# Performance work log

Hardware: AMD Instinct MI355X
Metric: run time of the kernel (lower is better)

The kernel has to match this reference:

```python
import jax, jax.numpy as jnp
import numpy as np

B, S, H, D = 1, 2048, 16, 128
CAUSAL = True


def setup_inputs() -> dict:
    key = jax.random.key(0)
    kq, kk, kv = jax.random.split(key, 3)
    query = jax.random.normal(kq, (B, S, H, D), dtype=jnp.float32)
    k_ = jax.random.normal(kk, (B, S, H, D), dtype=jnp.float32)
    v_ = jax.random.normal(kv, (B, S, H, D), dtype=jnp.float32)
    return {"query": query, "key": k_, "value": v_}


def reference(query, key, value):
    # Single-device equivalent of LongContextAttention:
    # Ulysses all-to-all and ring pass are identity on one rank; the math is
    # standard scaled-dot-product attention with flash-attn's default scale
    # softmax_scale = 1/sqrt(head_dim) and causal masking.
    d = query.shape[-1]
    scale = 1.0 / jnp.sqrt(jnp.asarray(d, dtype=query.dtype))
    # [B,S,H,D] x [B,T,H,D] -> [B,H,S,T]
    scores = jnp.einsum("bshd,bthd->bhst", query, key) * scale
    if CAUSAL:
        s, t = scores.shape[-2], scores.shape[-1]
        mask = jnp.tril(jnp.ones((s, t), dtype=bool))
        scores = jnp.where(mask, scores, jnp.finfo(scores.dtype).min)
    probs = jax.nn.softmax(scores, axis=-1)
    out = jnp.einsum("bhst,bthd->bshd", probs, value)
    return out
```

## Files before the change

### kernel.cpp

```cpp
#include <hip/hip_runtime.h>
#include <hip/hip_bf16.h>
#include <math.h>

#define SS 2048
#define HH 16
#define DD 128
#define HD (HH*DD)
#define QB 128
#define KVB 64

typedef __attribute__((ext_vector_type(8))) short bf16x8;
typedef __attribute__((ext_vector_type(16))) float f32x16;

__device__ __forceinline__ ushort f2bf(float f) {
  __hip_bfloat16 h = __float2bfloat16(f);
  return __builtin_bit_cast(ushort, h);
}
__device__ __forceinline__ uint pk2(float a, float b) {
  return ((uint)f2bf(b) << 16) | (uint)f2bf(a);
}
__device__ __forceinline__ float bf2f(ushort u) {
  uint x = ((uint)u) << 16;
  return __builtin_bit_cast(float, x);
}

__global__ __launch_bounds__(256, 2)
void attn_fwd(const float* __restrict__ Q, const float* __restrict__ K,
              const float* __restrict__ V,
              ushort* __restrict__ PO, float* __restrict__ PM,
              float* __restrict__ PL) {
  __shared__ alignas(16) ushort Klds[2][KVB * DD];
  __shared__ alignas(16) ushort VTlds[2][DD * KVB];

  const int tid  = threadIdx.x;
  const int lane = tid & 63;
  const int wid  = tid >> 6;
  const int q32  = lane & 31;
  const int hi   = lane >> 5;
  const int kxk  = (q32 & 15) << 4;
  const int kxv  = ((q32 & 7) << 4) ^ ((q32 & 8) << 1);

  const int g2   = (tid >> 4) & 3;
  const int n16  = tid & 15;
  const int dstg = wid * 16 + n16;
  const int swv  = ((dstg & 7) << 4) ^ ((dstg & 8) << 1);

  const int bx   = blockIdx.x;
  const int h    = bx & 15;
  const int rest = bx >> 4;
  const int pp   = rest >> 2;
  const int jj   = rest & 3;
  const int LA   = 2 * pp + 2;
  const int BND[5] = {0, 8, 17, 25, 34};
  const int tl = BND[jj], th = BND[jj + 1];

  const float SCALE = 1.44269504088896f / sqrtf((float)DD);
  const float* Kb = K + (size_t)h * DD;
  const float* Vb = V + (size_t)h * DD;

  uint4 kreg[4];
  uint2 vreg[2][4];

  auto loadt = [&](int t0) {
    #pragma unroll
    for (int it = 0; it < 4; ++it) {
      int e = tid + it * 256;
      int row = e >> 4, col = (e & 15) * 8;
      const float* src = &Kb[(size_t)(t0 + row) * HD + col];
      float4 a = *(const float4*)src;
      float4 b = *(const float4*)(src + 4);
      kreg[it].x = pk2(a.x, a.y); kreg[it].y = pk2(a.z, a.w);
      kreg[it].z = pk2(b.x, b.y); kreg[it].w = pk2(b.z, b.w);
    }
    #pragma unroll
    for (int half = 0; half < 2; ++half) {
      const int d = dstg + 64 * half;
      #pragma unroll
      for (int jv = 0; jv < 4; ++jv) {
        const int tt = 16 * jv + 4 * g2;
        const float* vp = &Vb[(size_t)(t0 + tt) * HD + d];
        vreg[half][jv].x = pk2(vp[0],      vp[HD]);
        vreg[half][jv].y = pk2(vp[2 * HD], vp[3 * HD]);
      }
    }
  };
  auto staget = [&](int b) {
    #pragma unroll
    for (int it = 0; it < 4; ++it) {
      int e = tid + it * 256;
      *(uint4*)((char*)&Klds[b][0] + ((e * 16) ^ (e & 0xF0))) = kreg[it];
    }
    #pragma unroll
    for (int half = 0; half < 2; ++half) {
      const int d = dstg + 64 * half;
      #pragma unroll
      for (int jv = 0; jv < 4; ++jv) {
        const int tt = 16 * jv + 4 * g2;
        *(uint2*)((char*)&VTlds[b][0] + ((d * 128 + tt * 2) ^ swv)) = vreg[half][jv];
      }
    }
  };

  for (int phase = 0; phase < 2; ++phase) {
    int qt, lo, hiT;
    if (phase == 0) { qt = pp;      lo = tl;               hiT = min(th, LA); }
    else            { qt = 15 - pp; lo = max(tl, LA) - LA; hiT = th - LA; }
    if (lo >= hiT) continue;

    const int qb = qt * QB;
    const int qw = qb + 32 * wid;
    const int qg = qw + q32;

    bf16x8 qf[8];
    {
      const float* qr = Q + ((size_t)qg * HH + h) * DD;
      #pragma unroll
      for (int ks = 0; ks < 8; ++ks) {
        float4 x = *(const float4*)&qr[16 * ks + 8 * hi];
        float4 y = *(const float4*)&qr[16 * ks + 8 * hi + 4];
        uint4 u;
        u.x = pk2(x.x * SCALE, x.y * SCALE);
        u.y = pk2(x.z * SCALE, x.w * SCALE);
        u.z = pk2(y.x * SCALE, y.y * SCALE);
        u.w = pk2(y.z * SCALE, y.w * SCALE);
        qf[ks] = __builtin_bit_cast(bf16x8, u);
      }
    }

    f32x16 acc[4];
    #pragma unroll
    for (int dt = 0; dt < 4; ++dt)
      #pragma unroll
      for (int e = 0; e < 16; ++e) acc[dt][e] = 0.f;
    float m = -1e30f, l = 0.f;

    loadt(lo * KVB);
    __syncthreads();
    staget(0);
    int cur = 0;

    for (int itile = lo; itile < hiT; ++itile) {
      __syncthreads();
      const bool more = (itile + 1 < hiT);
      if (more) loadt((itile + 1) * KVB);

      const int t0 = itile * KVB;
      const char* Kc = (const char*)&Klds[cur][0];
      const char* Vc = (const char*)&VTlds[cur][0];

      f32x16 s0, s1;
      #pragma unroll
      for (int e = 0; e < 16; ++e) { s0[e] = 0.f; s1[e] = 0.f; }
      __builtin_amdgcn_s_setprio(1);
      #pragma unroll
      for (int ks = 0; ks < 8; ++ks) {
        bf16x8 a0 = *(const bf16x8*)(Kc + ((q32 * 256 + 32 * ks + 16 * hi) ^ kxk));
        s0 = __builtin_amdgcn_mfma_f32_32x32x16_bf16(a0, qf[ks], s0, 0, 0, 0);
        bf16x8 a1 = *(const bf16x8*)(Kc + (((q32 + 32) * 256 + 32 * ks + 16 * hi) ^ kxk));
        s1 = __builtin_amdgcn_mfma_f32_32x32x16_bf16(a1, qf[ks], s1, 0, 0, 0);
      }
      __builtin_amdgcn_s_setprio(0);

      if (t0 + KVB - 1 > qw) {
        #pragma unroll
        for (int e = 0; e < 16; ++e) {
          int tloc = (e & 3) + 8 * (e >> 2) + 4 * hi;
          if (t0 + tloc > qg)      s0[e] = -INFINITY;
          if (t0 + 32 + tloc > qg) s1[e] = -INFINITY;
        }
      }

      float tmx[8];
      #pragma unroll
      for (int e = 0; e < 8; ++e)
        tmx[e] = fmaxf(fmaxf(s0[e], s0[e + 8]), fmaxf(s1[e], s1[e + 8]));
      #pragma unroll
      for (int st = 4; st >= 1; st >>= 1)
        #pragma unroll
        for (int e = 0; e < st; ++e) tmx[e] = fmaxf(tmx[e], tmx[e + st]);
      float mr = fmaxf(tmx[0], __shfl_xor(tmx[0], 32));

      if (!__all(mr <= m + 8.0f)) {
        float mn = fmaxf(m, mr);
        float corr = exp2f(m - mn);
        m = mn;
        l *= corr;
        #pragma unroll
        for (int dt = 0; dt < 4; ++dt)
          #pragma unroll
          for (int e = 0; e < 16; ++e) acc[dt][e] *= corr;
      }

      float ts[8];
      #pragma unroll
      for (int e = 0; e < 8; ++e) ts[e] = 0.f;
      #pragma unroll
      for (int e = 0; e < 16; ++e) {
        float p0 = exp2f(s0[e] - m); s0[e] = p0;
        float p1 = exp2f(s1[e] - m); s1[e] = p1;
        ts[e & 7] += p0 + p1;
      }
      #pragma unroll
      for (int st = 4; st >= 1; st >>= 1)
        #pragma unroll
        for (int e = 0; e < st; ++e) ts[e] += ts[e + st];
      float ps = ts[0] + __shfl_xor(ts[0], 32);
      l += ps;

      uint4 paf[4];
      #pragma unroll
      for (int tk = 0; tk < 4; ++tk) {
        float p0,p1,p2,p3,p4,p5,p6,p7;
        if (tk == 0) { p0=s0[0];p1=s0[1];p2=s0[2];p3=s0[3];p4=s0[4];p5=s0[5];p6=s0[6];p7=s0[7]; }
        else if (tk == 1) { p0=s0[8];p1=s0[9];p2=s0[10];p3=s0[11];p4=s0[12];p5=s0[13];p6=s0[14];p7=s0[15]; }
        else if (tk == 2) { p0=s1[0];p1=s1[1];p2=s1[2];p3=s1[3];p4=s1[4];p5=s1[5];p6=s1[6];p7=s1[7]; }
        else { p0=s1[8];p1=s1[9];p2=s1[10];p3=s1[11];p4=s1[12];p5=s1[13];p6=s1[14];p7=s1[15]; }
        uint A0 = pk2(p0, p1), A1 = pk2(p2, p3);
        uint B0 = pk2(p4, p5), B1 = pk2(p6, p7);
        uint x0 = hi ? A0 : B0, x1 = hi ? A1 : B1;
        uint r0 = (uint)__shfl_xor((int)x0, 32);
        uint r1 = (uint)__shfl_xor((int)x1, 32);
        paf[tk].x = hi ? r0 : A0;
        paf[tk].y = hi ? r1 : A1;
        paf[tk].z = hi ? B0 : r0;
        paf[tk].w = hi ? B1 : r1;
      }

      if (more) staget(cur ^ 1);

      __builtin_amdgcn_s_setprio(1);
      #pragma unroll
      for (int tk = 0; tk < 4; ++tk) {
        bf16x8 pb = __builtin_bit_cast(bf16x8, paf[tk]);
        #pragma unroll
        for (int dt = 0; dt < 4; ++dt) {
          bf16x8 va = *(const bf16x8*)(Vc +
                        (((dt * 32 + q32) * 128 + 32 * tk + 16 * hi) ^ kxv));
          acc[dt] = __builtin_amdgcn_mfma_f32_32x32x16_bf16(va, pb, acc[dt], 0, 0, 0);
        }
      }
      __builtin_amdgcn_s_setprio(0);

      cur ^= 1;
    }

    const int slot = (((h * 8 + pp) * 4 + jj) * 2) + phase;
    ushort* po = PO + (size_t)slot * (QB * DD);
    const int row = 32 * wid + q32;
    #pragma unroll
    for (int dt = 0; dt < 4; ++dt) {
      #pragma unroll
      for (int rq = 0; rq < 4; ++rq) {
        int d = 32 * dt + 8 * rq + 4 * hi;
        uint2 w;
        w.x = pk2(acc[dt][4 * rq + 0], acc[dt][4 * rq + 1]);
        w.y = pk2(acc[dt][4 * rq + 2], acc[dt][4 * rq + 3]);
        *(uint2*)&po[row * DD + d] = w;
      }
    }
    if (hi == 0) {
      PM[(size_t)slot * QB + row] = m;
      PL[(size_t)slot * QB + row] = l;
    }
  }
}

__global__ __launch_bounds__(256, 4)
void attn_merge(const ushort* __restrict__ PO, const float* __restrict__ PM,
                const float* __restrict__ PL, float* __restrict__ O) {
  const int bx  = blockIdx.x;
  const int h   = bx & 15;
  const int qt  = bx >> 4;
  const int tid = threadIdx.x;
  const int r   = tid >> 1;
  const int dh  = (tid & 1) * 64;

  const int BND[5] = {0, 8, 17, 25, 34};
  const int pp    = (qt < 8) ? qt : (15 - qt);
  const int phase = (qt < 8) ? 0 : 1;
  const int LA    = 2 * pp + 2;

  float mv[4], lv[4];
  float M = -1e30f;
  #pragma unroll
  for (int jj = 0; jj < 4; ++jj) {
    bool inc = (phase == 0) ? (BND[jj] < LA) : (BND[jj + 1] > LA);
    int slot = (((h * 8 + pp) * 4 + jj) * 2) + phase;
    mv[jj] = inc ? PM[(size_t)slot * QB + r] : -1e30f;
    lv[jj] = inc ? PL[(size_t)slot * QB + r] : 0.f;
    M = fmaxf(M, mv[jj]);
  }
  float L = 0.f;
  float o[64];
  #pragma unroll
  for (int k2 = 0; k2 < 64; ++k2) o[k2] = 0.f;
  #pragma unroll
  for (int jj = 0; jj < 4; ++jj) {
    bool inc = (phase == 0) ? (BND[jj] < LA) : (BND[jj + 1] > LA);
    if (!inc) continue;
    int slot = (((h * 8 + pp) * 4 + jj) * 2) + phase;
    float w = exp2f(mv[jj] - M);
    L += lv[jj] * w;
    const ushort* src = PO + (size_t)slot * (QB * DD) + r * DD + dh;
    #pragma unroll
    for (int k4 = 0; k4 < 16; ++k4) {
      ushort4 u = *(const ushort4*)&src[4 * k4];
      o[4*k4+0] += bf2f(u.x) * w;
      o[4*k4+1] += bf2f(u.y) * w;
      o[4*k4+2] += bf2f(u.z) * w;
      o[4*k4+3] += bf2f(u.w) * w;
    }
  }
  float inv = 1.0f / L;
  float* op = O + ((size_t)(qt * QB + r) * HH + h) * DD + dh;
  #pragma unroll
  for (int k4 = 0; k4 < 16; ++k4) {
    float4 x = make_float4(o[4*k4]*inv, o[4*k4+1]*inv, o[4*k4+2]*inv, o[4*k4+3]*inv);
    *(float4*)&op[4 * k4] = x;
  }
}

extern "C" void kernel_launch(void* const* d_in, const int* in_sizes, int n_in,
                              void* d_out, int out_size, void* d_ws, size_t ws_size,
                              hipStream_t stream) {
  const float* Q = (const float*)d_in[0];
  const float* K = (const float*)d_in[1];
  const float* V = (const float*)d_in[2];
  float* O = (float*)d_out;

  const size_t po_elems = (size_t)1024 * QB * DD;
  ushort* PO = (ushort*)d_ws;
  float*  PM = (float*)(PO + po_elems);
  float*  PL = PM + (size_t)1024 * QB;

  attn_fwd<<<dim3(512), 256, 0, stream>>>(Q, K, V, PO, PM, PL);
  attn_merge<<<dim3(256), 256, 0, stream>>>(PO, PM, PL, O);
}
```

Before: 64.57 us.

## Split causal KV range into fixed chunks with direct output for short rows

```diff
diff --git a/kernel.cpp b/kernel.cpp
--- a/kernel.cpp
+++ b/kernel.cpp
@@ -8,6 +8,8 @@
 #define HD (HH*DD)
 #define QB 128
 #define KVB 64
+#define CHUNK 6
+#define NJ 51
 
 typedef __attribute__((ext_vector_type(8))) short bf16x8;
 typedef __attribute__((ext_vector_type(16))) float f32x16;
@@ -23,14 +25,18 @@
   uint x = ((uint)u) << 16;
   return __builtin_bit_cast(float, x);
 }
-
-__global__ __launch_bounds__(256, 2)
+__device__ __forceinline__ int jbase(int q) {
+  int a = q / 3, b = q - 3 * a;
+  return (3 * a * (a + 1)) / 2 + b * (a + 1);
+}
+
+__global__ __launch_bounds__(256, 4)
 void attn_fwd(const float* __restrict__ Q, const float* __restrict__ K,
-              const float* __restrict__ V,
+              const float* __restrict__ V, float* __restrict__ O,
               ushort* __restrict__ PO, float* __restrict__ PM,
               float* __restrict__ PL) {
-  __shared__ alignas(16) ushort Klds[2][KVB * DD];
-  __shared__ alignas(16) ushort VTlds[2][DD * KVB];
+  __shared__ alignas(16) ushort Klds[KVB * DD];
+  __shared__ alignas(16) ushort VTlds[DD * KVB];
 
   const int tid  = threadIdx.x;
   const int lane = tid & 63;
@@ -45,14 +51,18 @@
   const int dstg = wid * 16 + n16;
   const int swv  = ((dstg & 7) << 4) ^ ((dstg & 8) << 1);
 
-  const int bx   = blockIdx.x;
-  const int h    = bx & 15;
-  const int rest = bx >> 4;
-  const int pp   = rest >> 2;
-  const int jj   = rest & 3;
-  const int LA   = 2 * pp + 2;
-  const int BND[5] = {0, 8, 17, 25, 34};
-  const int tl = BND[jj], th = BND[jj + 1];
+  const int bx = blockIdx.x;
+  const int h  = bx & 15;
+  const int j  = bx >> 4;
+  int qt = 0, c = 0;
+  for (int q2 = 15; q2 >= 0; --q2) {
+    int bq = jbase(q2);
+    if (j >= bq) { qt = q2; c = j - bq; break; }
+  }
+  const int nt  = 2 * qt + 2;
+  const int lo  = CHUNK * c;
+  const int hiT = min(lo + CHUNK, nt);
+  const int nc  = (qt + 3) / 3;
 
   const float SCALE = 1.44269504088896f / sqrtf((float)DD);
   const float* Kb = K + (size_t)h * DD;
@@ -84,11 +94,11 @@
       }
     }
   };
-  auto staget = [&](int b) {
+  auto staget = [&]() {
     #pragma unroll
     for (int it = 0; it < 4; ++it) {
       int e = tid + it * 256;
-      *(uint4*)((char*)&Klds[b][0] + ((e * 16) ^ (e & 0xF0))) = kreg[it];
+      *(uint4*)((char*)Klds + ((e * 16) ^ (e & 0xF0))) = kreg[it];
     }
     #pragma unroll
     for (int half = 0; half < 2; ++half) {
@@ -96,157 +106,160 @@
       #pragma unroll
       for (int jv = 0; jv < 4; ++jv) {
         const int tt = 16 * jv + 4 * g2;
-        *(uint2*)((char*)&VTlds[b][0] + ((d * 128 + tt * 2) ^ swv)) = vreg[half][jv];
+        *(uint2*)((char*)VTlds + ((d * 128 + tt * 2) ^ swv)) = vreg[half][jv];
       }
     }
   };
 
-  for (int phase = 0; phase < 2; ++phase) {
-    int qt, lo, hiT;
-    if (phase == 0) { qt = pp;      lo = tl;               hiT = min(th, LA); }
-    else            { qt = 15 - pp; lo = max(tl, LA) - LA; hiT = th - LA; }
-    if (lo >= hiT) continue;
-
-    const int qb = qt * QB;
-    const int qw = qb + 32 * wid;
-    const int qg = qw + q32;
-
-    bf16x8 qf[8];
-    {
-      const float* qr = Q + ((size_t)qg * HH + h) * DD;
-      #pragma unroll
-      for (int ks = 0; ks < 8; ++ks) {
-        float4 x = *(const float4*)&qr[16 * ks + 8 * hi];
-        float4 y = *(const float4*)&qr[16 * ks + 8 * hi + 4];
-        uint4 u;
-        u.x = pk2(x.x * SCALE, x.y * SCALE);
-        u.y = pk2(x.z * SCALE, x.w * SCALE);
-        u.z = pk2(y.x * SCALE, y.y * SCALE);
-        u.w = pk2(y.z * SCALE, y.w * SCALE);
-        qf[ks] = __builtin_bit_cast(bf16x8, u);
-      }
-    }
-
-    f32x16 acc[4];
-    #pragma unroll
-    for (int dt = 0; dt < 4; ++dt)
-      #pragma unroll
-      for (int e = 0; e < 16; ++e) acc[dt][e] = 0.f;
-    float m = -1e30f, l = 0.f;
-
-    loadt(lo * KVB);
+  const int qw = qt * QB + 32 * wid;
+  const int qg = qw + q32;
+
+  bf16x8 qf[8];
+  {
+    const float* qr = Q + ((size_t)qg * HH + h) * DD;
+    #pragma unroll
+    for (int ks = 0; ks < 8; ++ks) {
+      float4 x = *(const float4*)&qr[16 * ks + 8 * hi];
+      float4 y = *(const float4*)&qr[16 * ks + 8 * hi + 4];
+      uint4 u;
+      u.x = pk2(x.x * SCALE, x.y * SCALE);
+      u.y = pk2(x.z * SCALE, x.w * SCALE);
+      u.z = pk2(y.x * SCALE, y.y * SCALE);
+      u.w = pk2(y.z * SCALE, y.w * SCALE);
+      qf[ks] = __builtin_bit_cast(bf16x8, u);
+    }
+  }
+
+  f32x16 acc[4];
+  #pragma unroll
+  for (int dt = 0; dt < 4; ++dt)
+    #pragma unroll
+    for (int e = 0; e < 16; ++e) acc[dt][e] = 0.f;
+  float m = -1e30f, l = 0.f;
+
+  loadt(lo * KVB);
+  staget();
+
+  for (int itile = lo; itile < hiT; ++itile) {
     __syncthreads();
-    staget(0);
-    int cur = 0;
-
-    for (int itile = lo; itile < hiT; ++itile) {
-      __syncthreads();
-      const bool more = (itile + 1 < hiT);
-      if (more) loadt((itile + 1) * KVB);
-
-      const int t0 = itile * KVB;
-      const char* Kc = (const char*)&Klds[cur][0];
-      const char* Vc = (const char*)&VTlds[cur][0];
-
-      f32x16 s0, s1;
-      #pragma unroll
-      for (int e = 0; e < 16; ++e) { s0[e] = 0.f; s1[e] = 0.f; }
-      __builtin_amdgcn_s_setprio(1);
-      #pragma unroll
-      for (int ks = 0; ks < 8; ++ks) {
-        bf16x8 a0 = *(const bf16x8*)(Kc + ((q32 * 256 + 32 * ks + 16 * hi) ^ kxk));
-        s0 = __builtin_amdgcn_mfma_f32_32x32x16_bf16(a0, qf[ks], s0, 0, 0, 0);
-        bf16x8 a1 = *(const bf16x8*)(Kc + (((q32 + 32) * 256 + 32 * ks + 16 * hi) ^ kxk));
-        s1 = __builtin_amdgcn_mfma_f32_32x32x16_bf16(a1, qf[ks], s1, 0, 0, 0);
-      }
-      __builtin_amdgcn_s_setprio(0);
-
-      if (t0 + KVB - 1 > qw) {
+    const bool more = (itile + 1 < hiT);
+    if (more) loadt((itile + 1) * KVB);
+
+    const int t0 = itile * KVB;
+    const char* Kc = (const char*)Klds;
+    const char* Vc = (const char*)VTlds;
+
+    f32x16 s0, s1;
+    #pragma unroll
+    for (int e = 0; e < 16; ++e) { s0[e] = 0.f; s1[e] = 0.f; }
+    __builtin_amdgcn_s_setprio(1);
+    #pragma unroll
+    for (int ks = 0; ks < 8; ++ks) {
+      bf16x8 a0 = *(const bf16x8*)(Kc + ((q32 * 256 + 32 * ks + 16 * hi) ^ kxk));
+      s0 = __builtin_amdgcn_mfma_f32_32x32x16_bf16(a0, qf[ks], s0, 0, 0, 0);
+      bf16x8 a1 = *(const bf16x8*)(Kc + (((q32 + 32) * 256 + 32 * ks + 16 * hi) ^ kxk));
+      s1 = __builtin_amdgcn_mfma_f32_32x32x16_bf16(a1, qf[ks], s1, 0, 0, 0);
+    }
+    __builtin_amdgcn_s_setprio(0);
+
+    if (t0 + KVB - 1 > qw) {
+      #pragma unroll
+      for (int e = 0; e < 16; ++e) {
+        int tloc = (e & 3) + 8 * (e >> 2) + 4 * hi;
+        if (t0 + tloc > qg)      s0[e] = -INFINITY;
+        if (t0 + 32 + tloc > qg) s1[e] = -INFINITY;
+      }
+    }
+
+    float tmx[8];
+    #pragma unroll
+    for (int e = 0; e < 8; ++e)
+      tmx[e] = fmaxf(fmaxf(s0[e], s0[e + 8]), fmaxf(s1[e], s1[e + 8]));
+    #pragma unroll
+    for (int st = 4; st >= 1; st >>= 1)
+      #pragma unroll
+      for (int e = 0; e < st; ++e) tmx[e] = fmaxf(tmx[e], tmx[e + st]);
+    float mr = fmaxf(tmx[0], __shfl_xor(tmx[0], 32));
+
+    if (!__all(mr <= m + 8.0f)) {
+      float mn = fmaxf(m, mr);
+      float corr = exp2f(m - mn);
+      m = mn;
+      l *= corr;
+      #pragma unroll
+      for (int dt = 0; dt < 4; ++dt)
         #pragma unroll
-        for (int e = 0; e < 16; ++e) {
-          int tloc = (e & 3) + 8 * (e >> 2) + 4 * hi;
-          if (t0 + tloc > qg)      s0[e] = -INFINITY;
-          if (t0 + 32 + tloc > qg) s1[e] = -INFINITY;
-        }
-      }
-
-      float tmx[8];
-      #pragma unroll
-      for (int e = 0; e < 8; ++e)
-        tmx[e] = fmaxf(fmaxf(s0[e], s0[e + 8]), fmaxf(s1[e], s1[e + 8]));
-      #pragma unroll
-      for (int st = 4; st >= 1; st >>= 1)
-        #pragma unroll
-        for (int e = 0; e < st; ++e) tmx[e] = fmaxf(tmx[e], tmx[e + st]);
-      float mr = fmaxf(tmx[0], __shfl_xor(tmx[0], 32));
-
-      if (!__all(mr <= m + 8.0f)) {
-        float mn = fmaxf(m, mr);
-        float corr = exp2f(m - mn);
-        m = mn;
-        l *= corr;
-        #pragma unroll
-        for (int dt = 0; dt < 4; ++dt)
-          #pragma unroll
-          for (int e = 0; e < 16; ++e) acc[dt][e] *= corr;
-      }
-
-      float ts[8];
-      #pragma unroll
-      for (int e = 0; e < 8; ++e) ts[e] = 0.f;
-      #pragma unroll
-      for (int e = 0; e < 16; ++e) {
-        float p0 = exp2f(s0[e] - m); s0[e] = p0;
-        float p1 = exp2f(s1[e] - m); s1[e] = p1;
-        ts[e & 7] += p0 + p1;
-      }
-      #pragma unroll
-      for (int st = 4; st >= 1; st >>= 1)
-        #pragma unroll
-        for (int e = 0; e < st; ++e) ts[e] += ts[e + st];
-      float ps = ts[0] + __shfl_xor(ts[0], 32);
-      l += ps;
-
-      uint4 paf[4];
-      #pragma unroll
-      for (int tk = 0; tk < 4; ++tk) {
-        float p0,p1,p2,p3,p4,p5,p6,p7;
-        if (tk == 0) { p0=s0[0];p1=s0[1];p2=s0[2];p3=s0[3];p4=s0[4];p5=s0[5];p6=s0[6];p7=s0[7]; }
-        else if (tk == 1) { p0=s0[8];p1=s0[9];p2=s0[10];p3=s0[11];p4=s0[12];p5=s0[13];p6=s0[14];p7=s0[15]; }
-        else if (tk == 2) { p0=s1[0];p1=s1[1];p2=s1[2];p3=s1[3];p4=s1[4];p5=s1[5];p6=s1[6];p7=s1[7]; }
-        else { p0=s1[8];p1=s1[9];p2=s1[10];p3=s1[11];p4=s1[12];p5=s1[13];p6=s1[14];p7=s1[15]; }
-        uint A0 = pk2(p0, p1), A1 = pk2(p2, p3);
-        uint B0 = pk2(p4, p5), B1 = pk2(p6, p7);
-        uint x0 = hi ? A0 : B0, x1 = hi ? A1 : B1;
-        uint r0 = (uint)__shfl_xor((int)x0, 32);
-        uint r1 = (uint)__shfl_xor((int)x1, 32);
-        paf[tk].x = hi ? r0 : A0;
-        paf[tk].y = hi ? r1 : A1;
-        paf[tk].z = hi ? B0 : r0;
-        paf[tk].w = hi ? B1 : r1;
-      }
-
-      if (more) staget(cur ^ 1);
-
-      __builtin_amdgcn_s_setprio(1);
-      #pragma unroll
-      for (int tk = 0; tk < 4; ++tk) {
-        bf16x8 pb = __builtin_bit_cast(bf16x8, paf[tk]);
-        #pragma unroll
-        for (int dt = 0; dt < 4; ++dt) {
-          bf16x8 va = *(const bf16x8*)(Vc +
-                        (((dt * 32 + q32) * 128 + 32 * tk + 16 * hi) ^ kxv));
-          acc[dt] = __builtin_amdgcn_mfma_f32_32x32x16_bf16(va, pb, acc[dt], 0, 0, 0);
-        }
-      }
-      __builtin_amdgcn_s_setprio(0);
-
-      cur ^= 1;
-    }
-
-    const int slot = (((h * 8 + pp) * 4 + jj) * 2) + phase;
-    ushort* po = PO + (size_t)slot * (QB * DD);
-    const int row = 32 * wid + q32;
+        for (int e = 0; e < 16; ++e) acc[dt][e] *= corr;
+    }
+
+    float ts[8];
+    #pragma unroll
+    for (int e = 0; e < 8; ++e) ts[e] = 0.f;
+    #pragma unroll
+    for (int e = 0; e < 16; ++e) {
+      float p0 = exp2f(s0[e] - m); s0[e] = p0;
+      float p1 = exp2f(s1[e] - m); s1[e] = p1;
+      ts[e & 7] += p0 + p1;
+    }
+    #pragma unroll
+    for (int st = 4; st >= 1; st >>= 1)
+      #pragma unroll
+      for (int e = 0; e < st; ++e) ts[e] += ts[e + st];
+    float ps = ts[0] + __shfl_xor(ts[0], 32);
+    l += ps;
+
+    uint4 paf[4];
+    #pragma unroll
+    for (int tk = 0; tk < 4; ++tk) {
+      float p0,p1,p2,p3,p4,p5,p6,p7;
+      if (tk == 0) { p0=s0[0];p1=s0[1];p2=s0[2];p3=s0[3];p4=s0[4];p5=s0[5];p6=s0[6];p7=s0[7]; }
+      else if (tk == 1) { p0=s0[8];p1=s0[9];p2=s0[10];p3=s0[11];p4=s0[12];p5=s0[13];p6=s0[14];p7=s0[15]; }
+      else if (tk == 2) { p0=s1[0];p1=s1[1];p2=s1[2];p3=s1[3];p4=s1[4];p5=s1[5];p6=s1[6];p7=s1[7]; }
+      else { p0=s1[8];p1=s1[9];p2=s1[10];p3=s1[11];p4=s1[12];p5=s1[13];p6=s1[14];p7=s1[15]; }
+      uint A0 = pk2(p0, p1), A1 = pk2(p2, p3);
+      uint B0 = pk2(p4, p5), B1 = pk2(p6, p7);
+      uint x0 = hi ? A0 : B0, x1 = hi ? A1 : B1;
+      uint r0 = (uint)__shfl_xor((int)x0, 32);
+      uint r1 = (uint)__shfl_xor((int)x1, 32);
+      paf[tk].x = hi ? r0 : A0;
+      paf[tk].y = hi ? r1 : A1;
+      paf[tk].z = hi ? B0 : r0;
+      paf[tk].w = hi ? B1 : r1;
+    }
+
+    __builtin_amdgcn_s_setprio(1);
+    #pragma unroll
+    for (int tk = 0; tk < 4; ++tk) {
+      bf16x8 pb = __builtin_bit_cast(bf16x8, paf[tk]);
+      #pragma unroll
+      for (int dt = 0; dt < 4; ++dt) {
+        bf16x8 va = *(const bf16x8*)(Vc +
+                      (((dt * 32 + q32) * 128 + 32 * tk + 16 * hi) ^ kxv));
+        acc[dt] = __builtin_amdgcn_mfma_f32_32x32x16_bf16(va, pb, acc[dt], 0, 0, 0);
+      }
+    }
+    __builtin_amdgcn_s_setprio(0);
+
+    __syncthreads();
+    if (more) staget();
+  }
+
+  const int row = 32 * wid + q32;
+  if (nc == 1) {
+    float invl = 1.0f / l;
+    float* op = O + ((size_t)(qt * QB + row) * HH + h) * DD;
+    #pragma unroll
+    for (int dt = 0; dt < 4; ++dt) {
+      #pragma unroll
+      for (int rq = 0; rq < 4; ++rq) {
+        int d = 32 * dt + 8 * rq + 4 * hi;
+        float4 x = make_float4(acc[dt][4 * rq + 0] * invl, acc[dt][4 * rq + 1] * invl,
+                               acc[dt][4 * rq + 2] * invl, acc[dt][4 * rq + 3] * invl);
+        *(float4*)&op[d] = x;
+      }
+    }
+  } else {
+    ushort* po = PO + (size_t)bx * (QB * DD);
     #pragma unroll
     for (int dt = 0; dt < 4; ++dt) {
       #pragma unroll
@@ -259,8 +272,8 @@
       }
     }
     if (hi == 0) {
-      PM[(size_t)slot * QB + row] = m;
-      PL[(size_t)slot * QB + row] = l;
+      PM[(size_t)bx * QB + row] = m;
+      PL[(size_t)bx * QB + row] = l;
     }
   }
 }
@@ -270,37 +283,27 @@
                 const float* __restrict__ PL, float* __restrict__ O) {
   const int bx  = blockIdx.x;
   const int h   = bx & 15;
-  const int qt  = bx >> 4;
+  const int qt  = 3 + (bx >> 4);
   const int tid = threadIdx.x;
   const int r   = tid >> 1;
   const int dh  = (tid & 1) * 64;
 
-  const int BND[5] = {0, 8, 17, 25, 34};
-  const int pp    = (qt < 8) ? qt : (15 - qt);
-  const int phase = (qt < 8) ? 0 : 1;
-  const int LA    = 2 * pp + 2;
-
-  float mv[4], lv[4];
+  const int base = jbase(qt);
+  const int nc   = (qt + 3) / 3;
+
   float M = -1e30f;
-  #pragma unroll
-  for (int jj = 0; jj < 4; ++jj) {
-    bool inc = (phase == 0) ? (BND[jj] < LA) : (BND[jj + 1] > LA);
-    int slot = (((h * 8 + pp) * 4 + jj) * 2) + phase;
-    mv[jj] = inc ? PM[(size_t)slot * QB + r] : -1e30f;
-    lv[jj] = inc ? PL[(size_t)slot * QB + r] : 0.f;
-    M = fmaxf(M, mv[jj]);
+  for (int cc = 0; cc < nc; ++cc) {
+    int slot = (base + cc) * 16 + h;
+    M = fmaxf(M, PM[(size_t)slot * QB + r]);
   }
   float L = 0.f;
   float o[64];
   #pragma unroll
   for (int k2 = 0; k2 < 64; ++k2) o[k2] = 0.f;
-  #pragma unroll
-  for (int jj = 0; jj < 4; ++jj) {
-    bool inc = (phase == 0) ? (BND[jj] < LA) : (BND[jj + 1] > LA);
-    if (!inc) continue;
-    int slot = (((h * 8 + pp) * 4 + jj) * 2) + phase;
-    float w = exp2f(mv[jj] - M);
-    L += lv[jj] * w;
+  for (int cc = 0; cc < nc; ++cc) {
+    int slot = (base + cc) * 16 + h;
+    float w = exp2f(PM[(size_t)slot * QB + r] - M);
+    L += PL[(size_t)slot * QB + r] * w;
     const ushort* src = PO + (size_t)slot * (QB * DD) + r * DD + dh;
     #pragma unroll
     for (int k4 = 0; k4 < 16; ++k4) {
@@ -328,11 +331,11 @@
   const float* V = (const float*)d_in[2];
   float* O = (float*)d_out;
 
-  const size_t po_elems = (size_t)1024 * QB * DD;
+  const size_t po_elems = (size_t)(NJ * 16) * QB * DD;
   ushort* PO = (ushort*)d_ws;
   float*  PM = (float*)(PO + po_elems);
-  float*  PL = PM + (size_t)1024 * QB;
-
-  attn_fwd<<<dim3(512), 256, 0, stream>>>(Q, K, V, PO, PM, PL);
-  attn_merge<<<dim3(256), 256, 0, stream>>>(PO, PM, PL, O);
-}
+  float*  PL = PM + (size_t)(NJ * 16) * QB;
+
+  attn_fwd<<<dim3(NJ * 16), 256, 0, stream>>>(Q, K, V, O, PO, PM, PL);
+  attn_merge<<<dim3(13 * 16), 256, 0, stream>>>(PO, PM, PL, O);
+}
```

Measured after the change: 185.1 us. 187% more time.
